# Kernel tuning notes

Measured on AMD Instinct MI355X. Metric: run time of the kernel, lower is better.

The kernel has to match this reference:

```python
import jax, jax.numpy as jnp
import numpy as np

DIM = 3072
HEADS = 24
HD = 128
FF = 4 * DIM
EPS = 1e-6
SCALE_SHIFT = 1.0


def _ln(x):
    # LayerNorm, elementwise_affine=False
    mu = jnp.mean(x, axis=-1, keepdims=True)
    var = jnp.mean(jnp.square(x - mu), axis=-1, keepdims=True)
    return (x - mu) * jax.lax.rsqrt(var + EPS)


def _rms(x, w):
    # RMSNorm over head_dim with learned weight
    ms = jnp.mean(jnp.square(x), axis=-1, keepdims=True)
    return x * jax.lax.rsqrt(ms + EPS) * w


def _rope(x, cos, sin):
    # x: [B,S,H,D], cos/sin: [S,D]; interleaved rotate-half (diffusers style)
    xr = x.reshape(*x.shape[:-1], -1, 2)
    x1, x2 = xr[..., 0], xr[..., 1]
    rot = jnp.stack([-x2, x1], axis=-1).reshape(x.shape)
    return x * cos[None, :, None, :] + rot * sin[None, :, None, :]


def _mod_params(temb, w, b):
    m = jax.nn.silu(temb) @ w + b  # [B, 6*DIM]
    B = m.shape[0]
    m = m.reshape(B, -1, 6).transpose(0, 2, 1).reshape(B, -1)  # reorder to 6 blocks of DIM
    return jnp.split(m, 2, axis=-1)  # mod1, mod2 each [B, 3*DIM]


def _modulate(x, mp):
    shift, scale, gate = jnp.split(mp, 3, axis=-1)
    scale = scale + SCALE_SHIFT
    return x * scale[:, None, :] + shift[:, None, :], gate[:, None, :]


def setup_inputs() -> dict:
    key = jax.random.key(0)
    ks = jax.random.split(key, 32)
    B, ST, SI = 1, 512, 1024
    S = ST + SI
    r = lambda k, shp, s=1.0: jax.random.normal(k, shp, dtype=jnp.float32) * s
    W = 0.02  # weight init scale
    ang = jax.random.uniform(ks[5], (S, HD), minval=0.0, maxval=2 * np.pi)
    inp = {
        "hidden_states": r(ks[0], (B, SI, DIM)),
        "encoder_hidden_states": r(ks[1], (B, ST, DIM)),
        "encoder_hidden_states_mask": jnp.ones((B, ST), jnp.float32),
        "temb": r(ks[2], (B, DIM)),
        "rope_cos": jnp.cos(ang),
        "rope_sin": jnp.sin(ang),
        "w_img_mod": r(ks[6], (DIM, 6 * DIM), W), "b_img_mod": r(ks[7], (6 * DIM,), W),
        "w_txt_mod": r(ks[8], (DIM, 6 * DIM), W), "b_txt_mod": r(ks[9], (6 * DIM,), W),
        "norm_q_w": jnp.ones((HD,), jnp.float32), "norm_k_w": jnp.ones((HD,), jnp.float32),
        "norm_added_q_w": jnp.ones((HD,), jnp.float32), "norm_added_k_w": jnp.ones((HD,), jnp.float32),
        "w_qkv": r(ks[10], (DIM, 3 * DIM), W), "b_qkv": r(ks[11], (3 * DIM,), W),
        "w_add_qkv": r(ks[12], (DIM, 3 * DIM), W), "b_add_qkv": r(ks[13], (3 * DIM,), W),
        "w_out": r(ks[14], (DIM, DIM), W), "b_out": r(ks[15], (DIM,), W),
        "w_add_out": r(ks[16], (DIM, DIM), W), "b_add_out": r(ks[17], (DIM,), W),
        "w_img_mlp1": r(ks[18], (DIM, FF), W), "b_img_mlp1": r(ks[19], (FF,), W),
        "w_img_mlp2": r(ks[20], (FF, DIM), W), "b_img_mlp2": r(ks[21], (DIM,), W),
        "w_txt_mlp1": r(ks[22], (DIM, FF), W), "b_txt_mlp1": r(ks[23], (FF,), W),
        "w_txt_mlp2": r(ks[24], (FF, DIM), W), "b_txt_mlp2": r(ks[25], (DIM,), W),
    }
    return inp


def reference(hidden_states, encoder_hidden_states, encoder_hidden_states_mask, temb,
              rope_cos, rope_sin,
              w_img_mod, b_img_mod, w_txt_mod, b_txt_mod,
              norm_q_w, norm_k_w, norm_added_q_w, norm_added_k_w,
              w_qkv, b_qkv, w_add_qkv, b_add_qkv,
              w_out, b_out, w_add_out, b_add_out,
              w_img_mlp1, b_img_mlp1, w_img_mlp2, b_img_mlp2,
              w_txt_mlp1, b_txt_mlp1, w_txt_mlp2, b_txt_mlp2):
    B, SI, _ = hidden_states.shape
    ST = encoder_hidden_states.shape[1]

    img_mod1, img_mod2 = _mod_params(temb, w_img_mod, b_img_mod)
    txt_mod1, txt_mod2 = _mod_params(temb, w_txt_mod, b_txt_mod)

    img_m, img_g1 = _modulate(_ln(hidden_states), img_mod1)
    txt_m, txt_g1 = _modulate(_ln(encoder_hidden_states), txt_mod1)

    # joint attention
    iq, ik, iv = jnp.split(img_m @ w_qkv + b_qkv, 3, axis=-1)
    tq, tk, tv = jnp.split(txt_m @ w_add_qkv + b_add_qkv, 3, axis=-1)
    iq = _rms(iq.reshape(B, SI, HEADS, HD), norm_q_w)
    ik = _rms(ik.reshape(B, SI, HEADS, HD), norm_k_w)
    iv = iv.reshape(B, SI, HEADS, HD)
    tq = _rms(tq.reshape(B, ST, HEADS, HD), norm_added_q_w)
    tk = _rms(tk.reshape(B, ST, HEADS, HD), norm_added_k_w)
    tv = tv.reshape(B, ST, HEADS, HD)
    q = jnp.concatenate([tq, iq], axis=1)  # [B,S,H,D], txt first
    k = jnp.concatenate([tk, ik], axis=1)
    v = jnp.concatenate([tv, iv], axis=1)
    q = _rope(q, rope_cos, rope_sin)
    k = _rope(k, rope_cos, rope_sin)
    scores = jnp.einsum('bqhd,bkhd->bhqk', q, k) / np.float32(np.sqrt(HD))
    probs = jax.nn.softmax(scores, axis=-1)
    attn = jnp.einsum('bhqk,bkhd->bqhd', probs, v).reshape(B, ST + SI, HEADS * HD)

    txt_a = attn[:, :ST] @ w_add_out + b_add_out
    img_a = attn[:, ST:] @ w_out + b_out
    hidden = hidden_states + img_g1 * img_a
    enc = encoder_hidden_states + txt_g1 * txt_a

    # fused GELU(tanh) MLPs with modulation
    img_m2, img_g2 = _modulate(_ln(hidden), img_mod2)
    img_mlp = jax.nn.gelu(img_m2 @ w_img_mlp1 + b_img_mlp1, approximate=True) @ w_img_mlp2 + b_img_mlp2
    hidden = hidden + img_g2 * img_mlp

    txt_m2, txt_g2 = _modulate(_ln(enc), txt_mod2)
    txt_mlp = jax.nn.gelu(txt_m2 @ w_txt_mlp1 + b_txt_mlp1, approximate=True) @ w_txt_mlp2 + b_txt_mlp2
    enc = enc + txt_g2 * txt_mlp

    return enc, hidden
```

## Files before the change

kernel.cpp:

```cpp
#include <hip/hip_runtime.h>

#define DIMX 3072
#define STX 512
#define SIX 1024
#define SQX 1536
#define FFX 12288

typedef __attribute__((ext_vector_type(4))) float f32x4;
typedef __attribute__((ext_vector_type(8))) __bf16 bf16x8;
typedef __attribute__((ext_vector_type(4))) int i32x4;
typedef __attribute__((ext_vector_type(4))) unsigned short u16x4;

__device__ __forceinline__ unsigned short f2bf(float f){
  unsigned u = __builtin_bit_cast(unsigned, f);
  u += 0x7FFFu + ((u>>16)&1u);
  return (unsigned short)(u>>16);
}
__device__ __forceinline__ unsigned short usbf(float x){
  return __builtin_bit_cast(unsigned short, (__bf16)x);
}
__device__ __forceinline__ float bf2f(unsigned short h){
  unsigned u = ((unsigned)h)<<16;
  return __builtin_bit_cast(float, u);
}
__device__ __forceinline__ float gelu_tanh(float x){
  float x3 = x*x*x;
  float z = 0.7978845608028654f*(x + 0.044715f*x3);
  z = fminf(fmaxf(z, -15.f), 15.f);
  float e = exp2f(z*2.8853900817779268f);
  float th = (e-1.f)/(e+1.f);
  return 0.5f*x*(1.f+th);
}

__device__ __forceinline__ void gload16(const void* g, void* l){
  __builtin_amdgcn_global_load_lds(
      (const __attribute__((address_space(1))) void*)g,
      (__attribute__((address_space(3))) void*)l,
      16, 0, 0);
}


__global__ void k_silu(const float* __restrict__ temb, float* __restrict__ out){
  int i = blockIdx.x*256 + threadIdx.x;
  if(i < DIMX){
    float x = temb[i];
    out[i] = x / (1.f + exp2f(-x*1.4426950408889634f));
  }
}

__global__ void k_modinit(const float* __restrict__ b_img, const float* __restrict__ b_txt,
                          float* __restrict__ mod){
  int idx = blockIdx.x*256 + threadIdx.x;
  int mat = idx / 18432; int r = idx % 18432;
  int i = r/6, j = r%6;
  const float* b = mat ? b_txt : b_img;
  mod[mat*18432 + j*3072 + i] = b[r];
}

__global__ void k_modgemv(const float* __restrict__ w_img, const float* __restrict__ w_txt,
                          const float* __restrict__ silu_t, float* __restrict__ mod){
  int bz = blockIdx.x;
  int ks = bz & 7; bz >>= 3;
  int nc = bz % 18; int mat = bz / 18;
  const float* W = mat ? w_txt : w_img;
  __shared__ float st[384];
  int k0 = ks*384;
  for(int i = threadIdx.x; i < 384; i += 256) st[i] = silu_t[k0+i];
  __syncthreads();
  int n0 = nc*1024 + threadIdx.x*4;
  float ax=0.f, ay=0.f, az=0.f, aw=0.f;
  const float* Wp = W + (size_t)k0*18432 + n0;
  #pragma unroll 4
  for(int k=0;k<384;k++){
    float4 w = *(const float4*)(Wp + (size_t)k*18432);
    float s = st[k];
    ax += s*w.x; ay += s*w.y; az += s*w.z; aw += s*w.w;
  }
  float* md = mod + mat*18432;
  float vals[4] = {ax, ay, az, aw};
  #pragma unroll
  for(int j=0;j<4;j++){
    int n = n0+j; int i = n/6, jj = n%6;
    atomicAdd(&md[jj*3072 + i], vals[j]);
  }
}

__global__ void k_initC(float* __restrict__ out, const float* __restrict__ res,
                        const float* __restrict__ gate, const float* __restrict__ bias){
  int i = (blockIdx.x*256 + threadIdx.x)*4;
  int col = i % 3072;
  float4 r = *(const float4*)(res + i);
  float4 g = *(const float4*)(gate + col);
  float4 b = *(const float4*)(bias + col);
  float4 o = {r.x + g.x*b.x, r.y + g.y*b.y, r.z + g.z*b.z, r.w + g.w*b.w};
  *(float4*)(out + i) = o;
}

__global__ void k_lnmod(const float* __restrict__ x, const float* __restrict__ modp,
                        unsigned short* __restrict__ out){
  int row = blockIdx.x, t = threadIdx.x;
  const float* xr = x + (size_t)row*DIMX;
  float4 v0 = *(const float4*)(xr + t*4);
  float4 v1 = *(const float4*)(xr + 1024 + t*4);
  float4 v2 = *(const float4*)(xr + 2048 + t*4);
  float s  = v0.x+v0.y+v0.z+v0.w + v1.x+v1.y+v1.z+v1.w + v2.x+v2.y+v2.z+v2.w;
  float s2 = v0.x*v0.x+v0.y*v0.y+v0.z*v0.z+v0.w*v0.w
           + v1.x*v1.x+v1.y*v1.y+v1.z*v1.z+v1.w*v1.w
           + v2.x*v2.x+v2.y*v2.y+v2.z*v2.z+v2.w*v2.w;
  #pragma unroll
  for(int o=32;o>0;o>>=1){ s += __shfl_xor(s,o); s2 += __shfl_xor(s2,o); }
  __shared__ float rs_[4], rs2_[4];
  int wid = t>>6;
  if((t&63)==0){ rs_[wid]=s; rs2_[wid]=s2; }
  __syncthreads();
  float S  = rs_[0]+rs_[1]+rs_[2]+rs_[3];
  float S2 = rs2_[0]+rs2_[1]+rs2_[2]+rs2_[3];
  float mu = S*(1.f/3072.f);
  float var = S2*(1.f/3072.f) - mu*mu;
  float rstd = rsqrtf(var + 1e-6f);
  #pragma unroll
  for(int j=0;j<3;j++){
    int c = j*1024 + t*4;
    float4 sh = *(const float4*)(modp + c);
    float4 sc = *(const float4*)(modp + 3072 + c);
    float4 xv = (j==0)?v0:((j==1)?v1:v2);
    unsigned short h0 = f2bf((xv.x-mu)*rstd*(sc.x+1.f)+sh.x);
    unsigned short h1 = f2bf((xv.y-mu)*rstd*(sc.y+1.f)+sh.y);
    unsigned short h2 = f2bf((xv.z-mu)*rstd*(sc.z+1.f)+sh.z);
    unsigned short h3 = f2bf((xv.w-mu)*rstd*(sc.w+1.f)+sh.w);
    unsigned long long pk = (unsigned long long)(h0 | ((unsigned)h1<<16))
                          | ((unsigned long long)(h2 | ((unsigned)h3<<16))<<32);
    *(unsigned long long*)(out + (size_t)row*DIMX + c) = pk;
  }
}

__global__ void k_rmsrope(const unsigned short* __restrict__ qkv_txt,
                          const unsigned short* __restrict__ qkv_img,
                          const float* __restrict__ nqw, const float* __restrict__ nkw,
                          const float* __restrict__ naqw, const float* __restrict__ nakw,
                          const float* __restrict__ cosb, const float* __restrict__ sinb,
                          unsigned short* __restrict__ Q, unsigned short* __restrict__ K,
                          unsigned short* __restrict__ V){
  int s = blockIdx.x, h = blockIdx.y, t = threadIdx.x;
  bool txt = s < STX;
  const unsigned short* src = txt ? (qkv_txt + (size_t)s*9216)
                                  : (qkv_img + (size_t)(s-STX)*9216);
  const float* qw = txt ? naqw : nqw;
  const float* kw = txt ? nakw : nkw;
  int d0 = 2*t;
  float q1 = bf2f(src[h*128 + d0]),        q2 = bf2f(src[h*128 + d0 + 1]);
  float k1 = bf2f(src[3072 + h*128 + d0]), k2 = bf2f(src[3072 + h*128 + d0 + 1]);
  float v1 = bf2f(src[6144 + h*128 + d0]), v2 = bf2f(src[6144 + h*128 + d0 + 1]);
  float sq = q1*q1 + q2*q2, sk = k1*k1 + k2*k2;
  #pragma unroll
  for(int o=32;o>0;o>>=1){ sq += __shfl_xor(sq,o); sk += __shfl_xor(sk,o); }
  float rq = rsqrtf(sq*(1.f/128.f) + 1e-6f);
  float rk = rsqrtf(sk*(1.f/128.f) + 1e-6f);
  q1 *= rq*qw[d0]; q2 *= rq*qw[d0+1];
  k1 *= rk*kw[d0]; k2 *= rk*kw[d0+1];
  float c1 = cosb[(size_t)s*128 + d0], c2 = cosb[(size_t)s*128 + d0 + 1];
  float s1 = sinb[(size_t)s*128 + d0], s2 = sinb[(size_t)s*128 + d0 + 1];
  float Q1 = q1*c1 - q2*s1, Q2 = q2*c2 + q1*s2;
  float K1 = k1*c1 - k2*s1, K2 = k2*c2 + k1*s2;
  size_t o = ((size_t)s*24 + h)*128 + d0;
  Q[o] = f2bf(Q1); Q[o+1] = f2bf(Q2);
  K[o] = f2bf(K1); K[o+1] = f2bf(K2);
  V[o] = f2bf(v1); V[o+1] = f2bf(v2);
}

__global__ void k_vtrans(const unsigned short* __restrict__ V, unsigned short* __restrict__ VT){
  __shared__ unsigned short tile[64][136];
  int st = blockIdx.x, h = blockIdx.y, t = threadIdx.x;
  int s0 = st*64;
  {
    int s = t>>2;
    #pragma unroll
    for(int i=0;i<4;i++){
      int oct = ((t&3)<<2) + i;
      i32x4 d = *(const i32x4*)(V + ((size_t)(s0+s)*24 + h)*128 + oct*8);
      *(i32x4*)&tile[s][oct*8] = d;
    }
  }
  __syncthreads();
  {
    int d0 = t>>3; int strip = t&7;
    #pragma unroll
    for(int i=0;i<4;i++){
      int d = d0 + i*32;
      unsigned short h8[8];
      #pragma unroll
      for(int j=0;j<8;j++) h8[j] = tile[strip*8 + j][d];
      unsigned a0 = h8[0] | ((unsigned)h8[1]<<16);
      unsigned a1 = h8[2] | ((unsigned)h8[3]<<16);
      unsigned a2 = h8[4] | ((unsigned)h8[5]<<16);
      unsigned a3 = h8[6] | ((unsigned)h8[7]<<16);
      i32x4 dv = {(int)a0,(int)a1,(int)a2,(int)a3};
      *(i32x4*)(VT + ((size_t)h*128 + d)*1536 + s0 + strip*8) = dv;
    }
  }
}

__global__ __launch_bounds__(256,2) void k_fattn(
    const unsigned short* __restrict__ Q,
    const unsigned short* __restrict__ Kb,
    const unsigned short* __restrict__ VT,
    unsigned short* __restrict__ O)
{
  __shared__ unsigned short Kls[4][64][32];
  __shared__ unsigned short Vls[2][128][32];
  __shared__ unsigned short Pls[128][72];
  const int t = threadIdx.x;
  const int qb = blockIdx.x, h = blockIdx.y;
  const int lane = t&63, w = t>>6;
  const int lr = lane&15, lk = lane>>4;
  const float SC  = 0.08838834764831845f;
  const float L2E = 1.4426950408889634f;

  bf16x8 qf[2][4];
  {
    const unsigned short* qp = Q + ((size_t)(qb*128 + w*32 + lr)*3072) + h*128 + lk*8;
    #pragma unroll
    for(int mf=0;mf<2;mf++)
      #pragma unroll
      for(int ks=0;ks<4;ks++)
        qf[mf][ks] = *(const bf16x8*)(qp + (size_t)mf*16*3072 + ks*32);
  }

  f32x4 o[2][8];
  #pragma unroll
  for(int i=0;i<2;i++)
    #pragma unroll
    for(int j=0;j<8;j++) o[i][j] = (f32x4){0.f,0.f,0.f,0.f};
  float mrow[2][4], lrow[2][4];
  #pragma unroll
  for(int i=0;i<2;i++)
    #pragma unroll
    for(int r=0;r<4;r++){ mrow[i][r] = -3.0e30f; lrow[i][r] = 0.f; }

  for(int kv0=0; kv0<SQX; kv0+=64){
    __syncthreads();
    {
      const unsigned short* kp = Kb + ((size_t)(kv0 + (lane>>2))*3072) + h*128 + w*32 + (lane&3)*8;
      #pragma unroll
      for(int i=0;i<4;i++)
        gload16(kp + (size_t)i*16*3072, &Kls[w][i*16][0]);
    }
    {
      int c = w>>1;
      const unsigned short* vp = VT + ((size_t)(h*128 + (w&1)*64 + (lane>>2)))*1536 + kv0 + c*32 + (lane&3)*8;
      #pragma unroll
      for(int j=0;j<4;j++)
        gload16(vp + (size_t)j*16*1536, &Vls[c][(w&1)*64 + j*16][0]);
    }
    __syncthreads();

    f32x4 s[2][4];
    #pragma unroll
    for(int mf=0;mf<2;mf++)
      #pragma unroll
      for(int nf=0;nf<4;nf++) s[mf][nf] = (f32x4){0.f,0.f,0.f,0.f};
    #pragma unroll
    for(int ks=0;ks<4;ks++){
      bf16x8 kf[4];
      #pragma unroll
      for(int nf=0;nf<4;nf++) kf[nf] = *(const bf16x8*)&Kls[ks][nf*16+lr][lk*8];
      #pragma unroll
      for(int mf=0;mf<2;mf++)
        #pragma unroll
        for(int nf=0;nf<4;nf++)
          s[mf][nf] = __builtin_amdgcn_mfma_f32_16x16x32_bf16(qf[mf][ks], kf[nf], s[mf][nf], 0,0,0);
    }

    #pragma unroll
    for(int mf=0;mf<2;mf++){
      #pragma unroll
      for(int r=0;r<4;r++){
        float v = fmaxf(fmaxf(s[mf][0][r], s[mf][1][r]), fmaxf(s[mf][2][r], s[mf][3][r]));
        #pragma unroll
        for(int d=1; d<16; d<<=1) v = fmaxf(v, __shfl_xor(v, d));
        float nm = fmaxf(mrow[mf][r], v*SC);
        float fac = exp2f((mrow[mf][r]-nm)*L2E);
        mrow[mf][r] = nm;
        float rs = 0.f;
        #pragma unroll
        for(int nf=0;nf<4;nf++){
          float p = exp2f((s[mf][nf][r]*SC - nm)*L2E);
          s[mf][nf][r] = p;
          rs += p;
        }
        #pragma unroll
        for(int d=1; d<16; d<<=1) rs += __shfl_xor(rs, d);
        lrow[mf][r] = lrow[mf][r]*fac + rs;
        #pragma unroll
        for(int nf=0;nf<8;nf++) o[mf][nf][r] *= fac;
      }
    }

    #pragma unroll
    for(int mf=0;mf<2;mf++)
      #pragma unroll
      for(int nf=0;nf<4;nf++)
        #pragma unroll
        for(int r=0;r<4;r++)
          Pls[w*32 + mf*16 + lk*4 + r][nf*16 + lr] = usbf(s[mf][nf][r]);

    #pragma unroll
    for(int ks2=0; ks2<2; ks2++){
      bf16x8 pa[2];
      #pragma unroll
      for(int mf=0;mf<2;mf++)
        pa[mf] = *(const bf16x8*)&Pls[w*32 + mf*16 + lr][ks2*32 + lk*8];
      #pragma unroll
      for(int nf=0;nf<8;nf++){
        bf16x8 vf = *(const bf16x8*)&Vls[ks2][nf*16+lr][lk*8];
        #pragma unroll
        for(int mf=0;mf<2;mf++)
          o[mf][nf] = __builtin_amdgcn_mfma_f32_16x16x32_bf16(pa[mf], vf, o[mf][nf], 0,0,0);
      }
    }
  }

  #pragma unroll
  for(int mf=0;mf<2;mf++){
    float inv[4];
    #pragma unroll
    for(int r=0;r<4;r++) inv[r] = 1.f/lrow[mf][r];
    #pragma unroll
    for(int nf=0;nf<8;nf++){
      #pragma unroll
      for(int r=0;r<4;r++){
        size_t row = (size_t)qb*128 + w*32 + mf*16 + lk*4 + r;
        size_t col = (size_t)h*128 + nf*16 + lr;
        O[row*3072 + col] = usbf(o[mf][nf][r]*inv[r]);
      }
    }
  }
}

__global__ __launch_bounds__(256,4) void k_gemmW(
    const unsigned short* __restrict__ A, long lda,
    const float* __restrict__ W, long ldw,
    const float* __restrict__ bias,
    void* __restrict__ Cp, long ldc,
    int K, int KS, int mode,
    const float* __restrict__ gate)
{
  __shared__ unsigned short Als[2][128*32];
  __shared__ unsigned short Bls[2][128*40];
  const int t = threadIdx.x;
  const int bn = blockIdx.x, bm = blockIdx.y;
  const int zs = blockIdx.z;
  const int Kc = K / KS, kbeg = zs*Kc, kend = kbeg + Kc;

  const unsigned short* Ab = A + (size_t)bm*128*lda;
  const float* Wb = W + (size_t)bn*128;

  const int lane = t & 63, wid = t>>6, wr = wid>>1, wc = wid&1;
  const int lr = lane & 15, lk = lane>>4;
  const int srow = (lane>>2);
  const int soff = (lane&3)*8;
  const int wcb = (t&31)*4;
  const int wrb = (t>>5)*4;

  f32x4 acc[4][4];
  #pragma unroll
  for(int i=0;i<4;i++)
    #pragma unroll
    for(int j=0;j<4;j++) acc[i][j] = {0.f,0.f,0.f,0.f};

  float4 wreg[4];

  gload16(Ab + (size_t)(     wid*16 + srow)*lda + kbeg + soff, &Als[0][(     wid*16)*32]);
  gload16(Ab + (size_t)(64 + wid*16 + srow)*lda + kbeg + soff, &Als[0][(64 + wid*16)*32]);
  #pragma unroll
  for(int j=0;j<4;j++)
    wreg[j] = *(const float4*)(Wb + (size_t)(kbeg + wrb + j)*ldw + wcb);
  #pragma unroll
  for(int i=0;i<4;i++){
    u16x4 pk = { usbf(wreg[0][i]), usbf(wreg[1][i]), usbf(wreg[2][i]), usbf(wreg[3][i]) };
    *(u16x4*)&Bls[0][(wcb+i)*40 + wrb] = pk;
  }
  __syncthreads();

  unsigned short* AlsC = &Als[0][0]; unsigned short* AlsN = &Als[1][0];
  unsigned short* BlsC = &Bls[0][0]; unsigned short* BlsN = &Bls[1][0];

  for(int k0=kbeg; k0<kend; k0+=32){
    const bool has = (k0 + 32 < kend);
    if(has){
      int kn = k0 + 32;
      gload16(Ab + (size_t)(     wid*16 + srow)*lda + kn + soff, AlsN + (     wid*16)*32);
      gload16(Ab + (size_t)(64 + wid*16 + srow)*lda + kn + soff, AlsN + (64 + wid*16)*32);
      #pragma unroll
      for(int j=0;j<4;j++)
        wreg[j] = *(const float4*)(Wb + (size_t)(kn + wrb + j)*ldw + wcb);
    }
    {
      bf16x8 af[4], bfr[4];
      #pragma unroll
      for(int mf=0;mf<4;mf++) af[mf]  = *(const bf16x8*)&AlsC[(wr*64 + mf*16 + lr)*32 + lk*8];
      #pragma unroll
      for(int nf=0;nf<4;nf++) bfr[nf] = *(const bf16x8*)&BlsC[(wc*64 + nf*16 + lr)*40 + lk*8];
      #pragma unroll
      for(int mf=0;mf<4;mf++)
        #pragma unroll
        for(int nf=0;nf<4;nf++)
          acc[mf][nf] = __builtin_amdgcn_mfma_f32_16x16x32_bf16(af[mf], bfr[nf], acc[mf][nf], 0,0,0);
    }
    if(has){
      #pragma unroll
      for(int i=0;i<4;i++){
        u16x4 pk = { usbf(wreg[0][i]), usbf(wreg[1][i]), usbf(wreg[2][i]), usbf(wreg[3][i]) };
        *(u16x4*)&BlsN[(wcb+i)*40 + wrb] = pk;
      }
    }
    __syncthreads();
    unsigned short* tmp;
    tmp = AlsC; AlsC = AlsN; AlsN = tmp;
    tmp = BlsC; BlsC = BlsN; BlsN = tmp;
  }

  unsigned short* C16 = (unsigned short*)Cp;
  float* C32 = (float*)Cp;
  #pragma unroll
  for(int mf=0;mf<4;mf++){
    #pragma unroll
    for(int nf=0;nf<4;nf++){
      #pragma unroll
      for(int r=0;r<4;r++){
        size_t row = (size_t)bm*128 + wr*64 + mf*16 + lk*4 + r;
        size_t col = (size_t)bn*128 + wc*64 + nf*16 + lr;
        float v = acc[mf][nf][r];
        if(mode==0){
          C16[row*ldc + col] = f2bf(v + (bias ? bias[col] : 0.f));
        } else if(mode==1){
          C16[row*ldc + col] = f2bf(gelu_tanh(v + (bias ? bias[col] : 0.f)));
        } else {
          float g = gate ? gate[col] : 1.f;
          atomicAdd(&C32[row*ldc + col], g*v);
        }
      }
    }
  }
}


extern "C" void kernel_launch(void* const* d_in, const int* in_sizes, int n_in,
                              void* d_out, int out_size, void* d_ws, size_t ws_size,
                              hipStream_t stream){
  const float* hidden_states = (const float*)d_in[0];
  const float* enc_states    = (const float*)d_in[1];
  const float* temb          = (const float*)d_in[3];
  const float* rope_cos      = (const float*)d_in[4];
  const float* rope_sin      = (const float*)d_in[5];
  const float* w_img_mod     = (const float*)d_in[6];
  const float* b_img_mod     = (const float*)d_in[7];
  const float* w_txt_mod     = (const float*)d_in[8];
  const float* b_txt_mod     = (const float*)d_in[9];
  const float* norm_q_w      = (const float*)d_in[10];
  const float* norm_k_w      = (const float*)d_in[11];
  const float* norm_aq_w     = (const float*)d_in[12];
  const float* norm_ak_w     = (const float*)d_in[13];
  const float* w_qkv   = (const float*)d_in[14];
  const float* b_qkv   = (const float*)d_in[15];
  const float* w_aqkv  = (const float*)d_in[16];
  const float* b_aqkv  = (const float*)d_in[17];
  const float* w_out_  = (const float*)d_in[18];
  const float* b_out_  = (const float*)d_in[19];
  const float* w_aout  = (const float*)d_in[20];
  const float* b_aout  = (const float*)d_in[21];
  const float* w_mlp1i = (const float*)d_in[22];
  const float* b_mlp1i = (const float*)d_in[23];
  const float* w_mlp2i = (const float*)d_in[24];
  const float* b_mlp2i = (const float*)d_in[25];
  const float* w_mlp1t = (const float*)d_in[26];
  const float* b_mlp1t = (const float*)d_in[27];
  const float* w_mlp2t = (const float*)d_in[28];
  const float* b_mlp2t = (const float*)d_in[29];

  char* ws = (char*)d_ws;
  float* mod    = (float*)(ws + 0);
  float* silu_t = (float*)(ws + 147456);
  unsigned short* imgm = (unsigned short*)(ws + 159744);
  unsigned short* txtm = (unsigned short*)(ws + 6451200);
  float* hid = (float*)(ws + 9596928);
  float* enc = (float*)(ws + 22179840);
  unsigned short* Qb  = (unsigned short*)(ws + 47345664);
  unsigned short* Kb  = (unsigned short*)(ws + 56782848);
  unsigned short* Vb  = (unsigned short*)(ws + 66220032);
  unsigned short* attnb = (unsigned short*)(ws + 66220032);
  unsigned short* VTb = (unsigned short*)(ws + 75657216);
  unsigned short* qkvi = (unsigned short*)(ws + 141717504);
  unsigned short* qkvt = (unsigned short*)(ws + 160591872);
  unsigned short* mlph = (unsigned short*)(ws + 103968768);

  float* out_enc = (float*)d_out;
  float* out_hid = (float*)d_out + (size_t)STX*DIMX;

  k_silu<<<12,256,0,stream>>>(temb, silu_t);
  k_modinit<<<144,256,0,stream>>>(b_img_mod, b_txt_mod, mod);
  k_modgemv<<<288,256,0,stream>>>(w_img_mod, w_txt_mod, silu_t, mod);

  k_lnmod<<<SIX,256,0,stream>>>(hidden_states, mod + 0,     imgm);
  k_lnmod<<<STX,256,0,stream>>>(enc_states,    mod + 18432, txtm);

  k_gemmW<<<dim3(72,8,1),256,0,stream>>>(imgm,3072, w_qkv,9216, b_qkv,
      qkvi,9216, 3072,1, 0, nullptr);
  k_gemmW<<<dim3(72,4,1),256,0,stream>>>(txtm,3072, w_aqkv,9216, b_aqkv,
      qkvt,9216, 3072,1, 0, nullptr);

  k_rmsrope<<<dim3(1536,24),64,0,stream>>>(qkvt, qkvi, norm_q_w, norm_k_w,
      norm_aq_w, norm_ak_w, rope_cos, rope_sin, Qb, Kb, Vb);
  k_vtrans<<<dim3(24,24),256,0,stream>>>(Vb, VTb);

  k_fattn<<<dim3(12,24),256,0,stream>>>(Qb, Kb, VTb, attnb);

  k_initC<<<512*3,256,0,stream>>>(enc, enc_states, mod + 18432 + 2*3072, b_aout);
  k_initC<<<1024*3,256,0,stream>>>(hid, hidden_states, mod + 2*3072, b_out_);
  k_gemmW<<<dim3(24,4,8),256,0,stream>>>(attnb,3072, w_aout,3072, nullptr,
      enc,3072, 3072,8, 3, mod + 18432 + 2*3072);
  k_gemmW<<<dim3(24,8,4),256,0,stream>>>(attnb + (size_t)512*3072,3072, w_out_,3072, nullptr,
      hid,3072, 3072,4, 3, mod + 2*3072);

  k_lnmod<<<SIX,256,0,stream>>>(hid, mod + 3*3072, imgm);
  k_gemmW<<<dim3(96,8,1),256,0,stream>>>(imgm,3072, w_mlp1i,12288, b_mlp1i,
      mlph,12288, 3072,1, 1, nullptr);
  k_initC<<<1024*3,256,0,stream>>>(out_hid, hid, mod + 5*3072, b_mlp2i);
  k_gemmW<<<dim3(24,8,4),256,0,stream>>>(mlph,12288, w_mlp2i,3072, nullptr,
      out_hid,3072, 12288,4, 3, mod + 5*3072);

  k_lnmod<<<STX,256,0,stream>>>(enc, mod + 18432 + 3*3072, txtm);
  k_gemmW<<<dim3(96,4,1),256,0,stream>>>(txtm,3072, w_mlp1t,12288, b_mlp1t,
      mlph,12288, 3072,1, 1, nullptr);
  k_initC<<<512*3,256,0,stream>>>(out_enc, enc, mod + 18432 + 5*3072, b_mlp2t);
  k_gemmW<<<dim3(24,4,8),256,0,stream>>>(mlph,12288, w_mlp2t,3072, nullptr,
      out_enc,3072, 12288,8, 3, mod + 18432 + 5*3072);
}
```

Measured before the change: 1.195 ms.

## Batch img/txt streams into grouped kernels and swizzle LDS layouts

Merges the image and text LayerNorm-modulate, residual init, and all four GEMM pairs into single grouped launches that select operands by block row. This reduces launch count and improves GPU fill for the smaller text GEMMs, and gives the text MLP hidden state its own buffer. Separately, XOR swizzling is applied to the K/V tiles in flash attention and to the A/B tiles in the GEMM to reduce LDS bank conflicts. The text split-K factor changes from 8 to 4 as a side effect.

```diff
diff --git a/kernel.cpp b/kernel.cpp
--- a/kernel.cpp
+++ b/kernel.cpp
@@ -85,20 +85,33 @@
   }
 }
 
-__global__ void k_initC(float* __restrict__ out, const float* __restrict__ res,
-                        const float* __restrict__ gate, const float* __restrict__ bias){
-  int i = (blockIdx.x*256 + threadIdx.x)*4;
-  int col = i % 3072;
-  float4 r = *(const float4*)(res + i);
+__global__ void k_initC2(float* __restrict__ out0, const float* __restrict__ res0,
+                         const float* __restrict__ gate0, const float* __restrict__ bias0,
+                         float* __restrict__ out1, const float* __restrict__ res1,
+                         const float* __restrict__ gate1, const float* __restrict__ bias1,
+                         int R0){
+  long i = ((long)blockIdx.x*256 + threadIdx.x)*4;
+  int row = (int)(i / 3072);
+  int col = (int)(i % 3072);
+  const float* res; const float* gate; const float* bias; float* out;
+  long off;
+  if(row < R0){ res=res0; gate=gate0; bias=bias0; out=out0; off=i; }
+  else        { res=res1; gate=gate1; bias=bias1; out=out1; off=i - (long)R0*3072; }
+  float4 r = *(const float4*)(res + off);
   float4 g = *(const float4*)(gate + col);
   float4 b = *(const float4*)(bias + col);
   float4 o = {r.x + g.x*b.x, r.y + g.y*b.y, r.z + g.z*b.z, r.w + g.w*b.w};
-  *(float4*)(out + i) = o;
-}
-
-__global__ void k_lnmod(const float* __restrict__ x, const float* __restrict__ modp,
-                        unsigned short* __restrict__ out){
+  *(float4*)(out + off) = o;
+}
+
+__global__ void k_lnmod2(const float* __restrict__ x0, const float* __restrict__ modp0,
+                         unsigned short* __restrict__ out0,
+                         const float* __restrict__ x1, const float* __restrict__ modp1,
+                         unsigned short* __restrict__ out1, int R0){
   int row = blockIdx.x, t = threadIdx.x;
+  const float* x; const float* modp; unsigned short* out;
+  if(row < R0){ x=x0; modp=modp0; out=out0; }
+  else        { x=x1; modp=modp1; out=out1; row -= R0; }
   const float* xr = x + (size_t)row*DIMX;
   float4 v0 = *(const float4*)(xr + t*4);
   float4 v1 = *(const float4*)(xr + 1024 + t*4);
@@ -215,6 +228,8 @@
   const int lr = lane&15, lk = lane>>4;
   const float SC  = 0.08838834764831845f;
   const float L2E = 1.4426950408889634f;
+  const int schunk = ((lane&3) ^ ((lane>>2)&3))*8;
+  const int rswz   = ((lr&3)<<3);
 
   bf16x8 qf[2][4];
   {
@@ -240,14 +255,14 @@
   for(int kv0=0; kv0<SQX; kv0+=64){
     __syncthreads();
     {
-      const unsigned short* kp = Kb + ((size_t)(kv0 + (lane>>2))*3072) + h*128 + w*32 + (lane&3)*8;
+      const unsigned short* kp = Kb + ((size_t)(kv0 + (lane>>2))*3072) + h*128 + w*32 + schunk;
       #pragma unroll
       for(int i=0;i<4;i++)
         gload16(kp + (size_t)i*16*3072, &Kls[w][i*16][0]);
     }
     {
       int c = w>>1;
-      const unsigned short* vp = VT + ((size_t)(h*128 + (w&1)*64 + (lane>>2)))*1536 + kv0 + c*32 + (lane&3)*8;
+      const unsigned short* vp = VT + ((size_t)(h*128 + (w&1)*64 + (lane>>2)))*1536 + kv0 + c*32 + schunk;
       #pragma unroll
       for(int j=0;j<4;j++)
         gload16(vp + (size_t)j*16*1536, &Vls[c][(w&1)*64 + j*16][0]);
@@ -263,7 +278,7 @@
     for(int ks=0;ks<4;ks++){
       bf16x8 kf[4];
       #pragma unroll
-      for(int nf=0;nf<4;nf++) kf[nf] = *(const bf16x8*)&Kls[ks][nf*16+lr][lk*8];
+      for(int nf=0;nf<4;nf++) kf[nf] = *(const bf16x8*)&Kls[ks][nf*16+lr][(lk*8) ^ rswz];
       #pragma unroll
       for(int mf=0;mf<2;mf++)
         #pragma unroll
@@ -312,7 +327,7 @@
         pa[mf] = *(const bf16x8*)&Pls[w*32 + mf*16 + lr][ks2*32 + lk*8];
       #pragma unroll
       for(int nf=0;nf<8;nf++){
-        bf16x8 vf = *(const bf16x8*)&Vls[ks2][nf*16+lr][lk*8];
+        bf16x8 vf = *(const bf16x8*)&Vls[ks2][nf*16+lr][(lk*8) ^ rswz];
         #pragma unroll
         for(int mf=0;mf<2;mf++)
           o[mf][nf] = __builtin_amdgcn_mfma_f32_16x16x32_bf16(pa[mf], vf, o[mf][nf], 0,0,0);
@@ -338,17 +353,25 @@
 }
 
 __global__ __launch_bounds__(256,4) void k_gemmW(
-    const unsigned short* __restrict__ A, long lda,
-    const float* __restrict__ W, long ldw,
-    const float* __restrict__ bias,
-    void* __restrict__ Cp, long ldc,
-    int K, int KS, int mode,
-    const float* __restrict__ gate)
+    const unsigned short* __restrict__ A0, const unsigned short* __restrict__ A1, long lda,
+    const float* __restrict__ W0, const float* __restrict__ W1, long ldw,
+    const float* __restrict__ bias0, const float* __restrict__ bias1,
+    void* __restrict__ C0, void* __restrict__ C1, long ldc,
+    int nM0, int K, int KS, int mode,
+    const float* __restrict__ gate0, const float* __restrict__ gate1)
 {
   __shared__ unsigned short Als[2][128*32];
   __shared__ unsigned short Bls[2][128*40];
   const int t = threadIdx.x;
-  const int bn = blockIdx.x, bm = blockIdx.y;
+  const int bn = blockIdx.x;
+  int bm = blockIdx.y;
+  const bool sel1 = (bm >= nM0);
+  const unsigned short* A = sel1 ? A1 : A0;
+  const float* W  = sel1 ? W1 : W0;
+  const float* bias = sel1 ? bias1 : bias0;
+  const float* gate = sel1 ? gate1 : gate0;
+  void* Cp = sel1 ? C1 : C0;
+  if(sel1) bm -= nM0;
   const int zs = blockIdx.z;
   const int Kc = K / KS, kbeg = zs*Kc, kend = kbeg + Kc;
 
@@ -358,9 +381,11 @@
   const int lane = t & 63, wid = t>>6, wr = wid>>1, wc = wid&1;
   const int lr = lane & 15, lk = lane>>4;
   const int srow = (lane>>2);
-  const int soff = (lane&3)*8;
-  const int wcb = (t&31)*4;
-  const int wrb = (t>>5)*4;
+  const int soff = (((lane&3) ^ ((lane>>2)&3))*8);
+  const int aswz = (lk*8) ^ ((lr&3)<<3);
+  const int bswz = (lk*8) ^ (((lr>>2)&3)<<3);
+  const int u = t&31, v = t>>5;
+  const int wcol = (v*4) ^ ((u&3)<<3);
 
   f32x4 acc[4][4];
   #pragma unroll
@@ -374,11 +399,11 @@
   gload16(Ab + (size_t)(64 + wid*16 + srow)*lda + kbeg + soff, &Als[0][(64 + wid*16)*32]);
   #pragma unroll
   for(int j=0;j<4;j++)
-    wreg[j] = *(const float4*)(Wb + (size_t)(kbeg + wrb + j)*ldw + wcb);
+    wreg[j] = *(const float4*)(Wb + (size_t)(kbeg + v*4 + j)*ldw + u*4);
   #pragma unroll
   for(int i=0;i<4;i++){
     u16x4 pk = { usbf(wreg[0][i]), usbf(wreg[1][i]), usbf(wreg[2][i]), usbf(wreg[3][i]) };
-    *(u16x4*)&Bls[0][(wcb+i)*40 + wrb] = pk;
+    *(u16x4*)&Bls[0][(u*4+i)*40 + wcol] = pk;
   }
   __syncthreads();
 
@@ -393,14 +418,14 @@
       gload16(Ab + (size_t)(64 + wid*16 + srow)*lda + kn + soff, AlsN + (64 + wid*16)*32);
       #pragma unroll
       for(int j=0;j<4;j++)
-        wreg[j] = *(const float4*)(Wb + (size_t)(kn + wrb + j)*ldw + wcb);
+        wreg[j] = *(const float4*)(Wb + (size_t)(kn + v*4 + j)*ldw + u*4);
     }
     {
       bf16x8 af[4], bfr[4];
       #pragma unroll
-      for(int mf=0;mf<4;mf++) af[mf]  = *(const bf16x8*)&AlsC[(wr*64 + mf*16 + lr)*32 + lk*8];
-      #pragma unroll
-      for(int nf=0;nf<4;nf++) bfr[nf] = *(const bf16x8*)&BlsC[(wc*64 + nf*16 + lr)*40 + lk*8];
+      for(int mf=0;mf<4;mf++) af[mf]  = *(const bf16x8*)&AlsC[(wr*64 + mf*16 + lr)*32 + aswz];
+      #pragma unroll
+      for(int nf=0;nf<4;nf++) bfr[nf] = *(const bf16x8*)&BlsC[(wc*64 + nf*16 + lr)*40 + bswz];
       #pragma unroll
       for(int mf=0;mf<4;mf++)
         #pragma unroll
@@ -411,7 +436,7 @@
       #pragma unroll
       for(int i=0;i<4;i++){
         u16x4 pk = { usbf(wreg[0][i]), usbf(wreg[1][i]), usbf(wreg[2][i]), usbf(wreg[3][i]) };
-        *(u16x4*)&BlsN[(wcb+i)*40 + wrb] = pk;
+        *(u16x4*)&BlsN[(u*4+i)*40 + wcol] = pk;
       }
     }
     __syncthreads();
@@ -430,14 +455,14 @@
       for(int r=0;r<4;r++){
         size_t row = (size_t)bm*128 + wr*64 + mf*16 + lk*4 + r;
         size_t col = (size_t)bn*128 + wc*64 + nf*16 + lr;
-        float v = acc[mf][nf][r];
+        float v2 = acc[mf][nf][r];
         if(mode==0){
-          C16[row*ldc + col] = f2bf(v + (bias ? bias[col] : 0.f));
+          C16[row*ldc + col] = f2bf(v2 + (bias ? bias[col] : 0.f));
         } else if(mode==1){
-          C16[row*ldc + col] = f2bf(gelu_tanh(v + (bias ? bias[col] : 0.f)));
+          C16[row*ldc + col] = f2bf(gelu_tanh(v2 + (bias ? bias[col] : 0.f)));
         } else {
           float g = gate ? gate[col] : 1.f;
-          atomicAdd(&C32[row*ldc + col], g*v);
+          atomicAdd(&C32[row*ldc + col], g*v2);
         }
       }
     }
@@ -490,9 +515,10 @@
   unsigned short* Vb  = (unsigned short*)(ws + 66220032);
   unsigned short* attnb = (unsigned short*)(ws + 66220032);
   unsigned short* VTb = (unsigned short*)(ws + 75657216);
+  unsigned short* mlphI = (unsigned short*)(ws + 103968768);
+  unsigned short* mlphT = (unsigned short*)(ws + 129134592);
   unsigned short* qkvi = (unsigned short*)(ws + 141717504);
   unsigned short* qkvt = (unsigned short*)(ws + 160591872);
-  unsigned short* mlph = (unsigned short*)(ws + 103968768);
 
   float* out_enc = (float*)d_out;
   float* out_hid = (float*)d_out + (size_t)STX*DIMX;
@@ -501,13 +527,12 @@
   k_modinit<<<144,256,0,stream>>>(b_img_mod, b_txt_mod, mod);
   k_modgemv<<<288,256,0,stream>>>(w_img_mod, w_txt_mod, silu_t, mod);
 
-  k_lnmod<<<SIX,256,0,stream>>>(hidden_states, mod + 0,     imgm);
-  k_lnmod<<<STX,256,0,stream>>>(enc_states,    mod + 18432, txtm);
-
-  k_gemmW<<<dim3(72,8,1),256,0,stream>>>(imgm,3072, w_qkv,9216, b_qkv,
-      qkvi,9216, 3072,1, 0, nullptr);
-  k_gemmW<<<dim3(72,4,1),256,0,stream>>>(txtm,3072, w_aqkv,9216, b_aqkv,
-      qkvt,9216, 3072,1, 0, nullptr);
+  k_lnmod2<<<SQX,256,0,stream>>>(hidden_states, mod + 0, imgm,
+                                 enc_states, mod + 18432, txtm, SIX);
+
+  k_gemmW<<<dim3(72,12,1),256,0,stream>>>(imgm, txtm, 3072,
+      w_qkv, w_aqkv, 9216, b_qkv, b_aqkv,
+      qkvi, qkvt, 9216, 8, 3072,1, 0, nullptr,nullptr);
 
   k_rmsrope<<<dim3(1536,24),64,0,stream>>>(qkvt, qkvi, norm_q_w, norm_k_w,
       norm_aq_w, norm_ak_w, rope_cos, rope_sin, Qb, Kb, Vb);
@@ -515,24 +540,22 @@
 
   k_fattn<<<dim3(12,24),256,0,stream>>>(Qb, Kb, VTb, attnb);
 
-  k_initC<<<512*3,256,0,stream>>>(enc, enc_states, mod + 18432 + 2*3072, b_aout);
-  k_initC<<<1024*3,256,0,stream>>>(hid, hidden_states, mod + 2*3072, b_out_);
-  k_gemmW<<<dim3(24,4,8),256,0,stream>>>(attnb,3072, w_aout,3072, nullptr,
-      enc,3072, 3072,8, 3, mod + 18432 + 2*3072);
-  k_gemmW<<<dim3(24,8,4),256,0,stream>>>(attnb + (size_t)512*3072,3072, w_out_,3072, nullptr,
-      hid,3072, 3072,4, 3, mod + 2*3072);
-
-  k_lnmod<<<SIX,256,0,stream>>>(hid, mod + 3*3072, imgm);
-  k_gemmW<<<dim3(96,8,1),256,0,stream>>>(imgm,3072, w_mlp1i,12288, b_mlp1i,
-      mlph,12288, 3072,1, 1, nullptr);
-  k_initC<<<1024*3,256,0,stream>>>(out_hid, hid, mod + 5*3072, b_mlp2i);
-  k_gemmW<<<dim3(24,8,4),256,0,stream>>>(mlph,12288, w_mlp2i,3072, nullptr,
-      out_hid,3072, 12288,4, 3, mod + 5*3072);
-
-  k_lnmod<<<STX,256,0,stream>>>(enc, mod + 18432 + 3*3072, txtm);
-  k_gemmW<<<dim3(96,4,1),256,0,stream>>>(txtm,3072, w_mlp1t,12288, b_mlp1t,
-      mlph,12288, 3072,1, 1, nullptr);
-  k_initC<<<512*3,256,0,stream>>>(out_enc, enc, mod + 18432 + 5*3072, b_mlp2t);
-  k_gemmW<<<dim3(24,4,8),256,0,stream>>>(mlph,12288, w_mlp2t,3072, nullptr,
-      out_enc,3072, 12288,8, 3, mod + 18432 + 5*3072);
-}
+  k_initC2<<<4608,256,0,stream>>>(hid, hidden_states, mod + 2*3072, b_out_,
+                                  enc, enc_states, mod + 18432 + 2*3072, b_aout, SIX);
+  k_gemmW<<<dim3(24,12,4),256,0,stream>>>(attnb + (size_t)512*3072, attnb, 3072,
+      w_out_, w_aout, 3072, nullptr, nullptr,
+      hid, enc, 3072, 8, 3072,4, 3, mod + 2*3072, mod + 18432 + 2*3072);
+
+  k_lnmod2<<<SQX,256,0,stream>>>(hid, mod + 3*3072, imgm,
+                                 enc, mod + 18432 + 3*3072, txtm, SIX);
+
+  k_gemmW<<<dim3(96,12,1),256,0,stream>>>(imgm, txtm, 3072,
+      w_mlp1i, w_mlp1t, 12288, b_mlp1i, b_mlp1t,
+      mlphI, mlphT, 12288, 8, 3072,1, 1, nullptr,nullptr);
+
+  k_initC2<<<4608,256,0,stream>>>(out_hid, hid, mod + 5*3072, b_mlp2i,
+                                  out_enc, enc, mod + 18432 + 5*3072, b_mlp2t, SIX);
+  k_gemmW<<<dim3(24,12,4),256,0,stream>>>(mlphI, mlphT, 12288,
+      w_mlp2i, w_mlp2t, 3072, nullptr, nullptr,
+      out_hid, out_enc, 3072, 8, 12288,4, 3, mod + 5*3072, mod + 18432 + 5*3072);
+}
```

New measurement: 1.103 ms. 7.7% less time.
